# Performance work log

Measured on AMD Instinct MI355X. Metric: run time of the kernel, lower is better.

The kernel has to match this reference:

```python
import jax, jax.numpy as jnp
import numpy as np

DIM = 96
DIM_OUT = 96
NUM_HEADS = 1
HEAD_DIM = DIM_OUT // NUM_HEADS  # 96, also depthwise-conv channel count
STRIDE_Q = 1
STRIDE_KV = 2
EPS = 1e-6


def _layernorm(t, g, b):
    mu = jnp.mean(t, axis=-1, keepdims=True)
    var = jnp.mean(jnp.square(t - mu), axis=-1, keepdims=True)
    return (t - mu) * jax.lax.rsqrt(var + EPS) * g + b


def _depthwise(t_nchw, w, stride):
    # torch Conv2d(C, C, 3, stride, padding=1, groups=C, bias=False)
    # w: [C, 1, 3, 3]
    return jax.lax.conv_general_dilated(
        t_nchw, w, window_strides=(stride, stride), padding=[(1, 1), (1, 1)],
        feature_group_count=HEAD_DIM, dimension_numbers=('NCHW', 'OIHW', 'NCHW'))


def _attention_pool(t, w, stride, g, b, H, W):
    # t: [B, heads, L, C] -> pooled [B, heads, Lp, C]
    B, nh, L, C = t.shape
    t = t.reshape(B * nh, H, W, C).transpose(0, 3, 1, 2)  # [B*nh, C, H, W]
    t = _depthwise(t, w, stride)
    Hp, Wp = t.shape[2], t.shape[3]
    t = t.reshape(B, nh, C, Hp * Wp).transpose(0, 1, 3, 2)  # [B, nh, Lp, C]
    return _layernorm(t, g, b), Hp, Wp


def setup_inputs() -> dict:
    key = jax.random.key(0)
    ks = jax.random.split(key, 16)
    B, N = 32, 56 * 56
    inp = {
        'x': jax.random.normal(ks[0], (B, N, DIM), dtype=jnp.float32),
        'Wqkv': jax.random.normal(ks[1], (3 * DIM_OUT, DIM), dtype=jnp.float32) * 0.02,
        'bqkv': jax.random.normal(ks[2], (3 * DIM_OUT,), dtype=jnp.float32) * 0.02,
        'pool_q_w': jax.random.normal(ks[3], (HEAD_DIM, 1, 3, 3), dtype=jnp.float32) * 0.1,
        'gq': 1.0 + jax.random.normal(ks[4], (HEAD_DIM,), dtype=jnp.float32) * 0.02,
        'betq': jax.random.normal(ks[5], (HEAD_DIM,), dtype=jnp.float32) * 0.02,
        'pool_k_w': jax.random.normal(ks[6], (HEAD_DIM, 1, 3, 3), dtype=jnp.float32) * 0.1,
        'gk': 1.0 + jax.random.normal(ks[7], (HEAD_DIM,), dtype=jnp.float32) * 0.02,
        'betk': jax.random.normal(ks[8], (HEAD_DIM,), dtype=jnp.float32) * 0.02,
        'pool_v_w': jax.random.normal(ks[9], (HEAD_DIM, 1, 3, 3), dtype=jnp.float32) * 0.1,
        'gv': 1.0 + jax.random.normal(ks[10], (HEAD_DIM,), dtype=jnp.float32) * 0.02,
        'betv': jax.random.normal(ks[11], (HEAD_DIM,), dtype=jnp.float32) * 0.02,
        'Wproj': jax.random.normal(ks[12], (DIM_OUT, DIM_OUT), dtype=jnp.float32) * 0.02,
        'bproj': jax.random.normal(ks[13], (DIM_OUT,), dtype=jnp.float32) * 0.02,
        'h': 56,
        'w': 56,
    }
    return inp


def reference(x, Wqkv, bqkv, pool_q_w, gq, betq, pool_k_w, gk, betk,
              pool_v_w, gv, betv, Wproj, bproj, h, w):
    B, N, _ = x.shape
    qkv = (jnp.einsum('bnd,ed->bne', x, Wqkv) + bqkv)
    qkv = qkv.reshape(B, N, 3, NUM_HEADS, HEAD_DIM).transpose(2, 0, 3, 1, 4)
    q, k, v = qkv[0], qkv[1], qkv[2]  # each [B, heads, N, head_dim]

    q, Hq, Wq = _attention_pool(q, pool_q_w, STRIDE_Q, gq, betq, h, w)
    k, _, _ = _attention_pool(k, pool_k_w, STRIDE_KV, gk, betk, h, w)
    v, _, _ = _attention_pool(v, pool_v_w, STRIDE_KV, gv, betv, h, w)

    scale = HEAD_DIM ** -0.5
    attn = jax.nn.softmax(jnp.einsum('bhqc,bhkc->bhqk', q * scale, k), axis=-1)
    out = jnp.einsum('bhqk,bhkc->bhqc', attn, v) + q  # residual x + q
    out = out.transpose(0, 2, 1, 3).reshape(B, Hq * Wq, DIM_OUT)
    out = jnp.einsum('bnd,ed->bne', out, Wproj) + bproj
    return out
```

## Files before the change

### kernel.cpp

```cpp
#include <hip/hip_runtime.h>
#include <hip/hip_bf16.h>
#include <cmath>

#define BATCH 32
#define H_IN 56
#define W_IN 56
#define N_IN (H_IN * W_IN)
#define LKV 784
#define LKV_PAD 864
#define FRAG_ELEMS 82944

typedef short bf16x8 __attribute__((ext_vector_type(8)));
typedef float f32x4 __attribute__((ext_vector_type(4)));
typedef float f32x16 __attribute__((ext_vector_type(16)));

__device__ __forceinline__ unsigned pack_bf16(float a, float b) {
    unsigned ua = __builtin_bit_cast(unsigned, a);
    unsigned ub = __builtin_bit_cast(unsigned, b);
    ua = (ua + 0x7FFFu + ((ua >> 16) & 1u)) >> 16;
    ub = (ub + 0x7FFFu + ((ub >> 16) & 1u)) >> 16;
    return ua | (ub << 16);
}

__device__ __forceinline__ unsigned short cvt_bf16(float a) {
    unsigned ua = __builtin_bit_cast(unsigned, a);
    return (unsigned short)((ua + 0x7FFFu + ((ua >> 16) & 1u)) >> 16);
}

__device__ __forceinline__ float bf16_to_f32(unsigned short u) {
    unsigned v = ((unsigned)u) << 16;
    return __builtin_bit_cast(float, v);
}

__device__ __forceinline__ float bflo(unsigned u) {
    return __builtin_bit_cast(float, u << 16);
}
__device__ __forceinline__ float bfhi(unsigned u) {
    return __builtin_bit_cast(float, u & 0xFFFF0000u);
}

__device__ __forceinline__ unsigned pack_trunc(float a, float b) {
    return __builtin_amdgcn_perm(__builtin_bit_cast(unsigned, b),
                                 __builtin_bit_cast(unsigned, a), 0x07060302u);
}

__device__ __forceinline__ f32x16 zero16() {
    f32x16 z;
#pragma unroll
    for (int i = 0; i < 16; ++i) z[i] = 0.f;
    return z;
}

template <int NCT, bool IN_BF16, bool OUT_F32>
__global__ __launch_bounds__(256, 2) void gemm3_kernel(
    const void* __restrict__ Xv, const float* __restrict__ W,
    const float* __restrict__ bias, void* __restrict__ o0,
    void* __restrict__ o1, void* __restrict__ o2)
{
    __shared__ unsigned short Wl[NCT * 192 * 8];
    const int tid = threadIdx.x;
    const int wid = tid >> 6, lane = tid & 63;
    const int lo16 = lane & 15, hi = lane >> 4;

    for (int idx = tid; idx < NCT * 192; idx += 256) {
        int frag = idx >> 6, ln = idx & 63;
        int ct = frag / 3, kkb = frag % 3;
        int ch = ct * 16 + (ln & 15);
        int k0 = kkb * 32 + (ln >> 4) * 8;
        const float* s = W + ch * 96 + k0;
        float4 v0 = *reinterpret_cast<const float4*>(s);
        float4 v1 = *reinterpret_cast<const float4*>(s + 4);
        uint4 o;
        o.x = pack_bf16(v0.x, v0.y); o.y = pack_bf16(v0.z, v0.w);
        o.z = pack_bf16(v1.x, v1.y); o.w = pack_bf16(v1.z, v1.w);
        *reinterpret_cast<uint4*>(&Wl[idx * 8]) = o;
    }

    const size_t tok0 = (size_t)blockIdx.x * 128 + wid * 32;
    bf16x8 xb[6];
#pragma unroll
    for (int it = 0; it < 2; ++it) {
        size_t t = tok0 + it * 16 + lo16;
#pragma unroll
        for (int kkb = 0; kkb < 3; ++kkb) {
            if constexpr (IN_BF16) {
                xb[it * 3 + kkb] = *reinterpret_cast<const bf16x8*>(
                    (const unsigned short*)Xv + t * 96 + kkb * 32 + hi * 8);
            } else {
                const float* xp = (const float*)Xv + t * 96 + kkb * 32 + hi * 8;
                float4 a = *reinterpret_cast<const float4*>(xp);
                float4 c = *reinterpret_cast<const float4*>(xp + 4);
                uint4 u;
                u.x = pack_bf16(a.x, a.y); u.y = pack_bf16(a.z, a.w);
                u.z = pack_bf16(c.x, c.y); u.w = pack_bf16(c.z, c.w);
                xb[it * 3 + kkb] = __builtin_bit_cast(bf16x8, u);
            }
        }
    }
    __syncthreads();

#pragma unroll
    for (int ct = 0; ct < NCT; ++ct) {
        bf16x8 wf[3];
#pragma unroll
        for (int kkb = 0; kkb < 3; ++kkb)
            wf[kkb] = *reinterpret_cast<const bf16x8*>(&Wl[((ct * 3 + kkb) * 64 + lane) * 8]);
        const int chb = ct * 16 + hi * 4;
        float4 bv = *reinterpret_cast<const float4*>(bias + chb);
#pragma unroll
        for (int it = 0; it < 2; ++it) {
            f32x4 a = (f32x4){0.f, 0.f, 0.f, 0.f};
#pragma unroll
            for (int kkb = 0; kkb < 3; ++kkb)
                a = __builtin_amdgcn_mfma_f32_16x16x32_bf16(wf[kkb], xb[it * 3 + kkb], a, 0, 0, 0);
            size_t t = tok0 + it * 16 + lo16;
            float r0 = a[0] + bv.x, r1 = a[1] + bv.y;
            float r2 = a[2] + bv.z, r3 = a[3] + bv.w;
            if constexpr (OUT_F32) {
                *reinterpret_cast<float4*>((float*)o0 + t * 96 + chb) =
                    make_float4(r0, r1, r2, r3);
            } else {
                unsigned short* ob =
                    (unsigned short*)((ct < 6) ? o0 : (ct < 12 ? o1 : o2));
                int lch = (ct % 6) * 16 + hi * 4;
                uint2 p;
                p.x = pack_bf16(r0, r1);
                p.y = pack_bf16(r2, r3);
                *reinterpret_cast<uint2*>(ob + t * 96 + lch) = p;
            }
        }
    }
}

__global__ __launch_bounds__(192) void pool_all_kernel(
    const unsigned short* __restrict__ qin, const unsigned short* __restrict__ kin,
    const unsigned short* __restrict__ vin,
    const float* __restrict__ pqw, const float* __restrict__ pkw,
    const float* __restrict__ pvw,
    const float* __restrict__ gq, const float* __restrict__ betq,
    const float* __restrict__ gk, const float* __restrict__ betk,
    const float* __restrict__ gv, const float* __restrict__ betv,
    unsigned short* __restrict__ qout, unsigned short* __restrict__ kfr,
    unsigned short* __restrict__ vfr, float SC)
{
    __shared__ float wlds[864];
    __shared__ float2 part[192];
    __shared__ float2 mrs[16];

    int blk = blockIdx.x;
    const unsigned short* in; const float* wsrc; const float* g; const float* beta;
    unsigned short* out; int omode, stride, Wp, LpPad; float oscale;
    if (blk < 6272) {
        in = qin; wsrc = pqw; g = gq; beta = betq; out = qout;
        omode = 0; stride = 1; Wp = 56; LpPad = N_IN; oscale = 1.0f;
    } else if (blk < 8000) {
        blk -= 6272;
        in = kin; wsrc = pkw; g = gk; beta = betk; out = kfr;
        omode = 1; stride = 2; Wp = 28; LpPad = LKV_PAD; oscale = SC;
    } else {
        blk -= 8000;
        in = vin; wsrc = pvw; g = gv; beta = betv; out = vfr;
        omode = 2; stride = 2; Wp = 28; LpPad = LKV_PAD; oscale = 1.0f;
    }

    const int tid = threadIdx.x;
    for (int i = tid; i < 216; i += 192)
        *reinterpret_cast<float4*>(&wlds[i * 4]) =
            *reinterpret_cast<const float4*>(wsrc + i * 4);
    __syncthreads();

    const int tok_l = tid / 12, c8 = tid % 12;
    const int gt = blk * 16 + tok_l;
    const int Lp = (omode == 0) ? N_IN : LKV;
    const int b = gt / LpPad, rem = gt % LpPad;
    const bool pad = (rem >= Lp);
    const int yo = rem / Wp, xo = rem % Wp;

    float wt[9][8];
#pragma unroll
    for (int j = 0; j < 8; ++j) {
        const float* wr = &wlds[(c8 * 8 + j) * 9];
#pragma unroll
        for (int tap = 0; tap < 9; ++tap) wt[tap][j] = wr[tap];
    }

    float acc[8];
#pragma unroll
    for (int j = 0; j < 8; ++j) acc[j] = 0.f;

    const unsigned short* ib = in + (size_t)b * (H_IN * W_IN * 96) + c8 * 8;
#pragma unroll
    for (int dy = 0; dy < 3; ++dy) {
        const int iy = yo * stride + dy - 1;
        if ((unsigned)iy < (unsigned)H_IN) {
#pragma unroll
            for (int dx = 0; dx < 3; ++dx) {
                const int ix = xo * stride + dx - 1;
                if ((unsigned)ix < (unsigned)W_IN) {
                    const int tap = dy * 3 + dx;
                    uint4 d = *reinterpret_cast<const uint4*>(
                        ib + ((size_t)iy * W_IN + ix) * 96);
                    acc[0] += bflo(d.x) * wt[tap][0];
                    acc[1] += bfhi(d.x) * wt[tap][1];
                    acc[2] += bflo(d.y) * wt[tap][2];
                    acc[3] += bfhi(d.y) * wt[tap][3];
                    acc[4] += bflo(d.z) * wt[tap][4];
                    acc[5] += bfhi(d.z) * wt[tap][5];
                    acc[6] += bflo(d.w) * wt[tap][6];
                    acc[7] += bfhi(d.w) * wt[tap][7];
                }
            }
        }
    }

    float s = 0.f, s2 = 0.f;
#pragma unroll
    for (int j = 0; j < 8; ++j) { s += acc[j]; s2 += acc[j] * acc[j]; }
    part[tid] = make_float2(s, s2);
    __syncthreads();
    if (tid < 16) {
        float a = 0.f, q = 0.f;
#pragma unroll
        for (int j = 0; j < 12; ++j) {
            float2 p = part[tid * 12 + j];
            a += p.x; q += p.y;
        }
        float mu = a * (1.f / 96.f);
        float var = q * (1.f / 96.f) - mu * mu;
        mrs[tid] = make_float2(mu, rsqrtf(var + 1e-6f));
    }
    __syncthreads();
    const float mu = mrs[tok_l].x, rstd = mrs[tok_l].y;

    float4 g0 = *reinterpret_cast<const float4*>(g + c8 * 8);
    float4 g1 = *reinterpret_cast<const float4*>(g + c8 * 8 + 4);
    float4 b0 = *reinterpret_cast<const float4*>(beta + c8 * 8);
    float4 b1 = *reinterpret_cast<const float4*>(beta + c8 * 8 + 4);
    float r[8];
    r[0] = (acc[0] - mu) * rstd * (g0.x * oscale) + b0.x * oscale;
    r[1] = (acc[1] - mu) * rstd * (g0.y * oscale) + b0.y * oscale;
    r[2] = (acc[2] - mu) * rstd * (g0.z * oscale) + b0.z * oscale;
    r[3] = (acc[3] - mu) * rstd * (g0.w * oscale) + b0.w * oscale;
    r[4] = (acc[4] - mu) * rstd * (g1.x * oscale) + b1.x * oscale;
    r[5] = (acc[5] - mu) * rstd * (g1.y * oscale) + b1.y * oscale;
    r[6] = (acc[6] - mu) * rstd * (g1.z * oscale) + b1.z * oscale;
    r[7] = (acc[7] - mu) * rstd * (g1.w * oscale) + b1.w * oscale;
    if (omode != 0 && pad) {
#pragma unroll
        for (int j = 0; j < 8; ++j) r[j] = 0.f;
    }

    if (omode == 0) {
        uint4 o;
        o.x = pack_bf16(r[0], r[1]); o.y = pack_bf16(r[2], r[3]);
        o.z = pack_bf16(r[4], r[5]); o.w = pack_bf16(r[6], r[7]);
        *reinterpret_cast<uint4*>(out + (size_t)gt * 96 + c8 * 8) = o;
    } else if (omode == 1) {
        int t = rem >> 5, kkb = c8 >> 1, hi = c8 & 1;
        int ln = (rem & 31) | (hi << 5);
        uint4 o;
        o.x = pack_bf16(r[0], r[1]); o.y = pack_bf16(r[2], r[3]);
        o.z = pack_bf16(r[4], r[5]); o.w = pack_bf16(r[6], r[7]);
        *reinterpret_cast<uint4*>(out + (size_t)b * FRAG_ELEMS +
                                  ((size_t)(t * 6 + kkb) * 64 + ln) * 8) = o;
    } else {
        int kv16 = rem >> 4, e = rem & 7, lh = (rem >> 3) & 1;
#pragma unroll
        for (int j = 0; j < 8; ++j) {
            int j8 = c8 * 8 + j;
            int ct = j8 >> 5;
            int ln = (j8 & 31) | (lh << 5);
            out[(size_t)b * FRAG_ELEMS + ((size_t)(kv16 * 3 + ct) * 64 + ln) * 8 + e] =
                cvt_bf16(r[j]);
        }
    }
}

#define ATT_LOAD(KF, V0, V1, T)                                               \
    {                                                                         \
        _Pragma("unroll") for (int i_ = 0; i_ < 6; ++i_)                      \
            KF[i_] = *reinterpret_cast<const bf16x8*>(                        \
                Kb + ((size_t)((T) * 6 + i_) * 64 + lane) * 8);               \
        _Pragma("unroll") for (int c_ = 0; c_ < 3; ++c_) {                    \
            V0[c_] = *reinterpret_cast<const bf16x8*>(                        \
                Vb + ((size_t)((2 * (T)) * 3 + c_) * 64 + lane) * 8);         \
            V1[c_] = *reinterpret_cast<const bf16x8*>(                        \
                Vb + ((size_t)((2 * (T) + 1) * 3 + c_) * 64 + lane) * 8);     \
        }                                                                     \
    }

#define ATT_COMPUTE(KF, V0, V1, FULL)                                         \
    {                                                                         \
        f32x16 sE = zero16(), sO = zero16();                                  \
        sE = __builtin_amdgcn_mfma_f32_32x32x16_bf16(KF[0], qf[0], sE, 0, 0, 0); \
        sO = __builtin_amdgcn_mfma_f32_32x32x16_bf16(KF[1], qf[1], sO, 0, 0, 0); \
        sE = __builtin_amdgcn_mfma_f32_32x32x16_bf16(KF[2], qf[2], sE, 0, 0, 0); \
        sO = __builtin_amdgcn_mfma_f32_32x32x16_bf16(KF[3], qf[3], sO, 0, 0, 0); \
        sE = __builtin_amdgcn_mfma_f32_32x32x16_bf16(KF[4], qf[4], sE, 0, 0, 0); \
        sO = __builtin_amdgcn_mfma_f32_32x32x16_bf16(KF[5], qf[5], sO, 0, 0, 0); \
        float p[16];                                                          \
        _Pragma("unroll") for (int r_ = 0; r_ < 16; ++r_)                     \
            p[r_] = __builtin_amdgcn_exp2f(sE[r_] + sO[r_]);                  \
        float q0_ = 0.f, q1_ = 0.f;                                           \
        _Pragma("unroll") for (int r_ = 0; r_ < 8; ++r_) {                    \
            q0_ += p[r_]; q1_ += p[r_ + 8];                                   \
        }                                                                     \
        lsum += q0_ + ((FULL) ? q1_ : 0.f);                                   \
        unsigned d[8], sw[8];                                                 \
        _Pragma("unroll") for (int j_ = 0; j_ < 8; ++j_)                      \
            d[j_] = pack_trunc(p[2 * j_], p[2 * j_ + 1]);                     \
        _Pragma("unroll") for (int j_ = 0; j_ < 8; ++j_)                      \
            sw[j_] = (unsigned)__shfl_xor((int)d[j_], 32);                    \
        {                                                                     \
            int4 bi = h ? make_int4((int)sw[2], (int)sw[3], (int)d[2], (int)d[3]) \
                        : make_int4((int)d[0], (int)d[1], (int)sw[0], (int)sw[1]); \
            bf16x8 bf = __builtin_bit_cast(bf16x8, bi);                       \
            a0 = __builtin_amdgcn_mfma_f32_32x32x16_bf16(V0[0], bf, a0, 0, 0, 0); \
            a1 = __builtin_amdgcn_mfma_f32_32x32x16_bf16(V0[1], bf, a1, 0, 0, 0); \
            a2 = __builtin_amdgcn_mfma_f32_32x32x16_bf16(V0[2], bf, a2, 0, 0, 0); \
        }                                                                     \
        if (FULL) {                                                           \
            int4 bi = h ? make_int4((int)sw[6], (int)sw[7], (int)d[6], (int)d[7]) \
                        : make_int4((int)d[4], (int)d[5], (int)sw[4], (int)sw[5]); \
            bf16x8 bf = __builtin_bit_cast(bf16x8, bi);                       \
            a0 = __builtin_amdgcn_mfma_f32_32x32x16_bf16(V1[0], bf, a0, 0, 0, 0); \
            a1 = __builtin_amdgcn_mfma_f32_32x32x16_bf16(V1[1], bf, a1, 0, 0, 0); \
            a2 = __builtin_amdgcn_mfma_f32_32x32x16_bf16(V1[2], bf, a2, 0, 0, 0); \
        }                                                                     \
    }

__global__ __launch_bounds__(256) void attn_mfma8_kernel(
    const unsigned short* __restrict__ qpl, const unsigned short* __restrict__ Kf,
    const unsigned short* __restrict__ Vf, unsigned short* __restrict__ out)
{
    const int bid = blockIdx.x;
    const int wid = threadIdx.x >> 6;
    const int sblk = (bid & 7) * 98 + (bid >> 3);
    const int unit = sblk * 4 + wid;
    const int b = unit / 98, qblk = unit % 98;
    const int lane = threadIdx.x & 63;
    const int l31 = lane & 31, h = lane >> 5;

    const int qrow = qblk * 32 + l31;
    const unsigned short* qptr = qpl + ((size_t)b * N_IN + qrow) * 96;
    bf16x8 qf[6];
#pragma unroll
    for (int kkb = 0; kkb < 6; ++kkb)
        qf[kkb] = *reinterpret_cast<const bf16x8*>(qptr + kkb * 16 + h * 8);

    f32x16 a0 = zero16(), a1 = zero16(), a2 = zero16();
    float lsum = 0.f;

    const unsigned short* Kb = Kf + (size_t)b * FRAG_ELEMS;
    const unsigned short* Vb = Vf + (size_t)b * FRAG_ELEMS;

    bf16x8 kA[6], vA0[3], vA1[3];
    bf16x8 kB[6], vB0[3], vB1[3];

    ATT_LOAD(kA, vA0, vA1, 0);
    for (int t = 0; t < 24; t += 2) {
        ATT_LOAD(kB, vB0, vB1, t + 1);
        ATT_COMPUTE(kA, vA0, vA1, true);
        ATT_LOAD(kA, vA0, vA1, t + 2);
        ATT_COMPUTE(kB, vB0, vB1, true);
    }
    ATT_COMPUTE(kA, vA0, vA1, false);

    lsum += __shfl_xor(lsum, 32);
    const float inv = 1.f / lsum;

    unsigned short* op = out + ((size_t)b * N_IN + qrow) * 96;
#pragma unroll
    for (int ct = 0; ct < 3; ++ct) {
        const f32x16& a = (ct == 0) ? a0 : (ct == 1 ? a1 : a2);
#pragma unroll
        for (int gblk = 0; gblk < 4; ++gblk) {
            int ch = ct * 32 + gblk * 8 + 4 * h;
            ushort4 q4 = *reinterpret_cast<const ushort4*>(qptr + ch);
            uint2 pr;
            pr.x = pack_bf16(a[gblk * 4 + 0] * inv + bf16_to_f32(q4.x),
                             a[gblk * 4 + 1] * inv + bf16_to_f32(q4.y));
            pr.y = pack_bf16(a[gblk * 4 + 2] * inv + bf16_to_f32(q4.z),
                             a[gblk * 4 + 3] * inv + bf16_to_f32(q4.w));
            *reinterpret_cast<uint2*>(op + ch) = pr;
        }
    }
}

extern "C" void kernel_launch(void* const* d_in, const int* in_sizes, int n_in,
                              void* d_out, int out_size, void* d_ws, size_t ws_size,
                              hipStream_t stream)
{
    const float* x     = (const float*)d_in[0];
    const float* Wqkv  = (const float*)d_in[1];
    const float* bqkv  = (const float*)d_in[2];
    const float* pqw   = (const float*)d_in[3];
    const float* gq    = (const float*)d_in[4];
    const float* betq  = (const float*)d_in[5];
    const float* pkw   = (const float*)d_in[6];
    const float* gk    = (const float*)d_in[7];
    const float* betk  = (const float*)d_in[8];
    const float* pvw   = (const float*)d_in[9];
    const float* gv    = (const float*)d_in[10];
    const float* betv  = (const float*)d_in[11];
    const float* Wproj = (const float*)d_in[12];
    const float* bproj = (const float*)d_in[13];
    float* outp = (float*)d_out;

    char* ws = (char*)d_ws;
    const size_t QB    = (size_t)BATCH * N_IN * 96 * sizeof(short);
    const size_t FRAGB = (size_t)BATCH * FRAG_ELEMS * sizeof(short);
    unsigned short* qb   = (unsigned short*)(ws);
    unsigned short* kbuf = (unsigned short*)(ws + QB);
    unsigned short* vbuf = (unsigned short*)(ws + 2 * QB);
    unsigned short* qpb  = (unsigned short*)(ws + 3 * QB);
    unsigned short* Kfr  = (unsigned short*)(ws + 4 * QB);
    unsigned short* Vfr  = (unsigned short*)(ws + 4 * QB + FRAGB);
    unsigned short* attn_out = qb;

    const int T = BATCH * N_IN;

    const float SC = 0.1020620726159658f * 1.4426950408889634f;

    gemm3_kernel<18, false, false><<<T / 128, 256, 0, stream>>>(
        x, Wqkv, bqkv, qb, kbuf, vbuf);
    pool_all_kernel<<<9728, 192, 0, stream>>>(
        qb, kbuf, vbuf, pqw, pkw, pvw, gq, betq, gk, betk, gv, betv,
        qpb, Kfr, Vfr, SC);
    attn_mfma8_kernel<<<784, 256, 0, stream>>>(qpb, Kfr, Vfr, attn_out);
    gemm3_kernel<6, true, true><<<T / 128, 256, 0, stream>>>(
        attn_out, Wproj, bproj, outp, nullptr, nullptr);
}
```

Measured before the change: 151.4 us.

## Precompute bf16 weight fragments once, drop LDS staging, split attention into single-wave blocks

A new small kernel converts Wqkv and Wproj into bf16 MFMA fragment layout a single time. The GEMM kernels then read those fragments straight from global memory instead of having every block convert weights into LDS and wait at a barrier. The attention kernel becomes one wavefront per block with a swizzled block mapping, and its cross-half shuffles are computed lazily per fragment to cut live registers. This removes redundant per-block weight conversion and barriers, at the cost of an extra launch and weight reads through the cache instead of LDS.

After: 158.6 us. 4.8% more time.

```diff
diff --git a/kernel.cpp b/kernel.cpp
--- a/kernel.cpp
+++ b/kernel.cpp
@@ -51,30 +51,36 @@
     return z;
 }
 
+__global__ __launch_bounds__(256) void wprep_kernel(
+    const float* __restrict__ Wqkv, const float* __restrict__ Wproj,
+    unsigned short* __restrict__ wq, unsigned short* __restrict__ wp)
+{
+    int idx = blockIdx.x * 256 + threadIdx.x;
+    const float* src; unsigned short* dst; int li;
+    if (idx < 3456) { src = Wqkv; dst = wq; li = idx; }
+    else            { src = Wproj; dst = wp; li = idx - 3456; }
+    int frag = li >> 6, ln = li & 63;
+    int ct = frag / 3, kkb = frag % 3;
+    int ch = ct * 16 + (ln & 15);
+    int k0 = kkb * 32 + (ln >> 4) * 8;
+    const float* s = src + ch * 96 + k0;
+    float4 v0 = *reinterpret_cast<const float4*>(s);
+    float4 v1 = *reinterpret_cast<const float4*>(s + 4);
+    uint4 o;
+    o.x = pack_bf16(v0.x, v0.y); o.y = pack_bf16(v0.z, v0.w);
+    o.z = pack_bf16(v1.x, v1.y); o.w = pack_bf16(v1.z, v1.w);
+    *reinterpret_cast<uint4*>(dst + (size_t)li * 8) = o;
+}
+
 template <int NCT, bool IN_BF16, bool OUT_F32>
-__global__ __launch_bounds__(256, 2) void gemm3_kernel(
-    const void* __restrict__ Xv, const float* __restrict__ W,
+__global__ __launch_bounds__(256) void gemm4_kernel(
+    const void* __restrict__ Xv, const unsigned short* __restrict__ Wfr,
     const float* __restrict__ bias, void* __restrict__ o0,
     void* __restrict__ o1, void* __restrict__ o2)
 {
-    __shared__ unsigned short Wl[NCT * 192 * 8];
     const int tid = threadIdx.x;
     const int wid = tid >> 6, lane = tid & 63;
     const int lo16 = lane & 15, hi = lane >> 4;
-
-    for (int idx = tid; idx < NCT * 192; idx += 256) {
-        int frag = idx >> 6, ln = idx & 63;
-        int ct = frag / 3, kkb = frag % 3;
-        int ch = ct * 16 + (ln & 15);
-        int k0 = kkb * 32 + (ln >> 4) * 8;
-        const float* s = W + ch * 96 + k0;
-        float4 v0 = *reinterpret_cast<const float4*>(s);
-        float4 v1 = *reinterpret_cast<const float4*>(s + 4);
-        uint4 o;
-        o.x = pack_bf16(v0.x, v0.y); o.y = pack_bf16(v0.z, v0.w);
-        o.z = pack_bf16(v1.x, v1.y); o.w = pack_bf16(v1.z, v1.w);
-        *reinterpret_cast<uint4*>(&Wl[idx * 8]) = o;
-    }
 
     const size_t tok0 = (size_t)blockIdx.x * 128 + wid * 32;
     bf16x8 xb[6];
@@ -97,14 +103,14 @@
             }
         }
     }
-    __syncthreads();
 
 #pragma unroll
     for (int ct = 0; ct < NCT; ++ct) {
         bf16x8 wf[3];
 #pragma unroll
         for (int kkb = 0; kkb < 3; ++kkb)
-            wf[kkb] = *reinterpret_cast<const bf16x8*>(&Wl[((ct * 3 + kkb) * 64 + lane) * 8]);
+            wf[kkb] = *reinterpret_cast<const bf16x8*>(
+                Wfr + ((size_t)(ct * 3 + kkb) * 64 + lane) * 8);
         const int chb = ct * 16 + hi * 4;
         float4 bv = *reinterpret_cast<const float4*>(bias + chb);
 #pragma unroll
@@ -276,6 +282,17 @@
     }
 }
 
+#define MAKE_BI(BI, D0, D1, D2, D3)                                           \
+    int4 BI;                                                                  \
+    {                                                                         \
+        unsigned s0_ = (unsigned)__shfl_xor((int)(D0), 32);                   \
+        unsigned s1_ = (unsigned)__shfl_xor((int)(D1), 32);                   \
+        unsigned s2_ = (unsigned)__shfl_xor((int)(D2), 32);                   \
+        unsigned s3_ = (unsigned)__shfl_xor((int)(D3), 32);                   \
+        BI = h ? make_int4((int)s2_, (int)s3_, (int)(D2), (int)(D3))          \
+               : make_int4((int)(D0), (int)(D1), (int)s0_, (int)s1_);         \
+    }
+
 #define ATT_LOAD(KF, V0, V1, T)                                               \
     {                                                                         \
         _Pragma("unroll") for (int i_ = 0; i_ < 6; ++i_)                      \
@@ -306,22 +323,18 @@
             q0_ += p[r_]; q1_ += p[r_ + 8];                                   \
         }                                                                     \
         lsum += q0_ + ((FULL) ? q1_ : 0.f);                                   \
-        unsigned d[8], sw[8];                                                 \
+        unsigned d[8];                                                        \
         _Pragma("unroll") for (int j_ = 0; j_ < 8; ++j_)                      \
             d[j_] = pack_trunc(p[2 * j_], p[2 * j_ + 1]);                     \
-        _Pragma("unroll") for (int j_ = 0; j_ < 8; ++j_)                      \
-            sw[j_] = (unsigned)__shfl_xor((int)d[j_], 32);                    \
         {                                                                     \
-            int4 bi = h ? make_int4((int)sw[2], (int)sw[3], (int)d[2], (int)d[3]) \
-                        : make_int4((int)d[0], (int)d[1], (int)sw[0], (int)sw[1]); \
+            MAKE_BI(bi, d[0], d[1], d[2], d[3]);                              \
             bf16x8 bf = __builtin_bit_cast(bf16x8, bi);                       \
             a0 = __builtin_amdgcn_mfma_f32_32x32x16_bf16(V0[0], bf, a0, 0, 0, 0); \
             a1 = __builtin_amdgcn_mfma_f32_32x32x16_bf16(V0[1], bf, a1, 0, 0, 0); \
             a2 = __builtin_amdgcn_mfma_f32_32x32x16_bf16(V0[2], bf, a2, 0, 0, 0); \
         }                                                                     \
         if (FULL) {                                                           \
-            int4 bi = h ? make_int4((int)sw[6], (int)sw[7], (int)d[6], (int)d[7]) \
-                        : make_int4((int)d[4], (int)d[5], (int)sw[4], (int)sw[5]); \
+            MAKE_BI(bi, d[4], d[5], d[6], d[7]);                              \
             bf16x8 bf = __builtin_bit_cast(bf16x8, bi);                       \
             a0 = __builtin_amdgcn_mfma_f32_32x32x16_bf16(V1[0], bf, a0, 0, 0, 0); \
             a1 = __builtin_amdgcn_mfma_f32_32x32x16_bf16(V1[1], bf, a1, 0, 0, 0); \
@@ -329,16 +342,14 @@
         }                                                                     \
     }
 
-__global__ __launch_bounds__(256) void attn_mfma8_kernel(
+__global__ __launch_bounds__(64) void attn_mfma10_kernel(
     const unsigned short* __restrict__ qpl, const unsigned short* __restrict__ Kf,
     const unsigned short* __restrict__ Vf, unsigned short* __restrict__ out)
 {
     const int bid = blockIdx.x;
-    const int wid = threadIdx.x >> 6;
-    const int sblk = (bid & 7) * 98 + (bid >> 3);
-    const int unit = sblk * 4 + wid;
-    const int b = unit / 98, qblk = unit % 98;
-    const int lane = threadIdx.x & 63;
+    const int swz = (bid & 7) * 392 + (bid >> 3);
+    const int b = swz / 98, qblk = swz % 98;
+    const int lane = threadIdx.x;
     const int l31 = lane & 31, h = lane >> 5;
 
     const int qrow = qblk * 32 + l31;
@@ -416,18 +427,21 @@
     unsigned short* qpb  = (unsigned short*)(ws + 3 * QB);
     unsigned short* Kfr  = (unsigned short*)(ws + 4 * QB);
     unsigned short* Vfr  = (unsigned short*)(ws + 4 * QB + FRAGB);
+    unsigned short* wqf  = (unsigned short*)(ws + 4 * QB + 2 * FRAGB);
+    unsigned short* wpf  = (unsigned short*)(ws + 4 * QB + 2 * FRAGB + 56320);
     unsigned short* attn_out = qb;
 
     const int T = BATCH * N_IN;
 
     const float SC = 0.1020620726159658f * 1.4426950408889634f;
 
-    gemm3_kernel<18, false, false><<<T / 128, 256, 0, stream>>>(
-        x, Wqkv, bqkv, qb, kbuf, vbuf);
+    wprep_kernel<<<18, 256, 0, stream>>>(Wqkv, Wproj, wqf, wpf);
+    gemm4_kernel<18, false, false><<<T / 128, 256, 0, stream>>>(
+        x, wqf, bqkv, qb, kbuf, vbuf);
     pool_all_kernel<<<9728, 192, 0, stream>>>(
         qb, kbuf, vbuf, pqw, pkw, pvw, gq, betq, gk, betk, gv, betv,
         qpb, Kfr, Vfr, SC);
-    attn_mfma8_kernel<<<784, 256, 0, stream>>>(qpb, Kfr, Vfr, attn_out);
-    gemm3_kernel<6, true, true><<<T / 128, 256, 0, stream>>>(
-        attn_out, Wproj, bproj, outp, nullptr, nullptr);
-}
+    attn_mfma10_kernel<<<3136, 64, 0, stream>>>(qpb, Kfr, Vfr, attn_out);
+    gemm4_kernel<6, true, true><<<T / 128, 256, 0, stream>>>(
+        attn_out, wpf, bproj, outp, nullptr, nullptr);
+}
```
